# Performance work log

Measured on AMD Instinct MI355X. Metric: run time of the kernel, lower is better.

## Reference

```python
import jax, jax.numpy as jnp
import numpy as np
import math

N, C, W, H = 8, 1024, 1024, 16
D = C // H  # head size = 64


def setup_inputs() -> dict:
    key = jax.random.key(0)
    ks = jax.random.split(key, 7)
    s = 1.0 / math.sqrt(C)
    return {
        "hidden_states": jax.random.normal(ks[0], (N, C, W), jnp.float32),
        "attention_mask": jnp.zeros((N, 1, 1, W), jnp.float32),
        "wq": jax.random.normal(ks[1], (C, C), jnp.float32) * s,
        "bq": jax.random.normal(ks[2], (C,), jnp.float32) * 0.02,
        "wk": jax.random.normal(ks[3], (C, C), jnp.float32) * s,
        "bk": jax.random.normal(ks[4], (C,), jnp.float32) * 0.02,
        "wv": jax.random.normal(ks[5], (C, C), jnp.float32) * s,
        "bv": jax.random.normal(ks[6], (C,), jnp.float32) * 0.02,
    }


def reference(hidden_states, attention_mask, wq, bq, wk, bk, wv, bv):
    # conv1d(kernel=1, groups=1) == per-position GEMM: [N,C,W] x [Cout,Cin] -> [N,Cout,W]
    q = jnp.einsum('ncw,oc->now', hidden_states, wq) + bq[None, :, None]
    k = jnp.einsum('ncw,oc->now', hidden_states, wk) + bk[None, :, None]
    v = jnp.einsum('ncw,oc->now', hidden_states, wv) + bv[None, :, None]
    # split heads: [N,C,W] -> [N,H,D,W]
    q = q.reshape(N, H, D, W).transpose(0, 1, 3, 2)  # [N,H,W,D]
    k = k.reshape(N, H, D, W)                         # [N,H,D,W]
    v = v.reshape(N, H, D, W).transpose(0, 1, 3, 2)  # [N,H,W,D]
    scores = jnp.einsum('nhqd,nhdk->nhqk', q, k) / math.sqrt(D)
    scores = scores + attention_mask  # broadcast [N,1,1,W]
    probs = jax.nn.softmax(scores, axis=-1)
    ctx = jnp.einsum('nhqk,nhkd->nhqd', probs, v)    # [N,H,W,D]
    # merge heads back to [N,C,W]
    return ctx.transpose(0, 1, 3, 2).reshape(N, C, W)
```

## Files before the change

kernel.cpp:

```cpp
#include <hip/hip_runtime.h>
#include <hip/hip_bf16.h>

typedef __bf16 bf16x8 __attribute__((ext_vector_type(8)));
typedef __bf16 bf16x4 __attribute__((ext_vector_type(4)));
typedef float f32x4 __attribute__((ext_vector_type(4)));

#define N_ 8
#define C_ 1024
#define W_ 1024
#define H_ 16
#define D_ 64

typedef __attribute__((address_space(3))) void lds_void;
typedef const __attribute__((address_space(1))) void gbl_void;
static __device__ __forceinline__ void gload_lds16(const void* g, void* l) {
    __builtin_amdgcn_global_load_lds((gbl_void*)g, (lds_void*)l, 16, 0, 0);
}

__global__ __launch_bounds__(256)
void convert_w(const float* __restrict__ s0, const float* __restrict__ s1,
               const float* __restrict__ s2, __bf16* __restrict__ dst) {
    const float* s = blockIdx.y == 0 ? s0 : (blockIdx.y == 1 ? s1 : s2);
    __bf16* d = dst + (long)blockIdx.y * C_ * C_;
    const long i = ((long)blockIdx.x * 256 + threadIdx.x) * 8;
    f32x4 a = *(const f32x4*)(const void*)(s + i);
    f32x4 b = *(const f32x4*)(const void*)(s + i + 4);
    bf16x8 v;
    #pragma unroll
    for (int t = 0; t < 4; ++t) { v[t] = (__bf16)a[t]; v[t + 4] = (__bf16)b[t]; }
    *(bf16x8*)(void*)(d + i) = v;
}

__global__ __launch_bounds__(256)
void transpose_x(const float* __restrict__ in, __bf16* __restrict__ outp) {
    __shared__ float tile[64][68];
    const long bin  = (long)blockIdx.z * C_ * W_;
    const long bout = (long)blockIdx.z * W_ * C_;
    const int w0 = blockIdx.x * 64, c0 = blockIdx.y * 64;
    const int t = threadIdx.x;
    const int rr = t >> 4;
    const int cg = (t & 15) * 4;
    #pragma unroll
    for (int it = 0; it < 4; ++it) {
        const int cr = it * 16 + rr;
        f32x4 v = *(const f32x4*)(const void*)(in + bin + (long)(c0 + cr) * W_ + w0 + cg);
        *(f32x4*)&tile[cr][cg] = v;
    }
    __syncthreads();
    #pragma unroll
    for (int it = 0; it < 4; ++it) {
        const int wr = it * 16 + rr;
        bf16x4 o;
        #pragma unroll
        for (int u = 0; u < 4; ++u) o[u] = (__bf16)tile[cg + u][wr];
        *(bf16x4*)(void*)(outp + bout + (long)(w0 + wr) * C_ + c0 + cg) = o;
    }
}

template<int OUT_T>
static __device__ __forceinline__
void gemm_body(const __bf16* __restrict__ Aw, const __bf16* __restrict__ Xn,
               const float* __restrict__ bias, __bf16* __restrict__ Pn,
               const int o0, const int w0,
               __bf16* __restrict__ As, __bf16* __restrict__ Bs) {
    constexpr int BK = 64;
    const int tid = threadIdx.x;
    const int wv = tid >> 6, lane = tid & 63;
    const int l15 = lane & 15, quad = lane >> 4;
    const int wr = (wv >> 1) * 64, wc = (wv & 1) * 64;
    const int lr8 = lane >> 3;
    const int lp = lane & 7;

    f32x4 acc[4][4] = {};

    for (int k0 = 0; k0 < C_; k0 += BK) {
        #pragma unroll
        for (int j = 0; j < 4; ++j) {
            const int seg = wv * 4 + j;
            const int r = seg * 8 + lr8;
            const int q = lp ^ (r & 7);
            gload_lds16(Aw + (long)(o0 + r) * C_ + k0 + q * 8, As + seg * 512);
            gload_lds16(Xn + (long)(w0 + r) * C_ + k0 + q * 8, Bs + seg * 512);
        }
        __syncthreads();
        bf16x8 af[4][2], bf[4][2];
        #pragma unroll
        for (int mt = 0; mt < 4; ++mt) {
            const int R = wr + mt * 16 + l15;
            #pragma unroll
            for (int s = 0; s < 2; ++s) {
                const int pos = (s * 4 + quad) ^ (R & 7);
                af[mt][s] = *(const bf16x8*)(const void*)&As[R * 64 + pos * 8];
            }
        }
        #pragma unroll
        for (int nt = 0; nt < 4; ++nt) {
            const int R = wc + nt * 16 + l15;
            #pragma unroll
            for (int s = 0; s < 2; ++s) {
                const int pos = (s * 4 + quad) ^ (R & 7);
                bf[nt][s] = *(const bf16x8*)(const void*)&Bs[R * 64 + pos * 8];
            }
        }
        #pragma unroll
        for (int s = 0; s < 2; ++s)
            #pragma unroll
            for (int mt = 0; mt < 4; ++mt)
                #pragma unroll
                for (int nt = 0; nt < 4; ++nt) {
                    if (OUT_T == 0)
                        acc[mt][nt] = __builtin_amdgcn_mfma_f32_16x16x32_bf16(af[mt][s], bf[nt][s], acc[mt][nt], 0, 0, 0);
                    else
                        acc[mt][nt] = __builtin_amdgcn_mfma_f32_16x16x32_bf16(bf[nt][s], af[mt][s], acc[mt][nt], 0, 0, 0);
                }
        __syncthreads();
    }

    #pragma unroll
    for (int mt = 0; mt < 4; ++mt) {
        #pragma unroll
        for (int nt = 0; nt < 4; ++nt) {
            #pragma unroll
            for (int rg = 0; rg < 4; ++rg) {
                if (OUT_T == 0) {
                    const int col = w0 + wc + nt * 16 + l15;
                    const int row = o0 + wr + mt * 16 + quad * 4 + rg;
                    Pn[(long)row * W_ + col] = (__bf16)(acc[mt][nt][rg] + bias[row]);
                } else {
                    const int o = o0 + wr + mt * 16 + l15;
                    const int w = w0 + wc + nt * 16 + quad * 4 + rg;
                    Pn[(long)w * C_ + o] = (__bf16)(acc[mt][nt][rg] + bias[o]);
                }
            }
        }
    }
}

__global__ __launch_bounds__(256)
void gemm_qkv(const __bf16* __restrict__ Wb, const __bf16* __restrict__ Xt,
              const float* __restrict__ bq, const float* __restrict__ bk,
              const float* __restrict__ bv,
              __bf16* __restrict__ Qt, __bf16* __restrict__ Kt,
              __bf16* __restrict__ Vb) {
    __shared__ __align__(16) __bf16 As[128 * 64];
    __shared__ __align__(16) __bf16 Bs[128 * 64];
    const int f = blockIdx.x;
    const int n = f & 7;
    const int j = f >> 3;
    const int which = j >> 6;
    const int t = j & 63;
    const int o0 = (t >> 3) * 128;
    const int w0 = (t & 7) * 128;
    const size_t SZ = (size_t)C_ * W_;
    const size_t WSZ = (size_t)C_ * C_;
    const __bf16* Xn = Xt + (size_t)n * SZ;
    const __bf16* Aw = Wb + (size_t)which * WSZ;
    if (which < 2)
        gemm_body<1>(Aw, Xn, which ? bk : bq, (which ? Kt : Qt) + n * SZ, o0, w0, As, Bs);
    else
        gemm_body<0>(Aw, Xn, bv, Vb + n * SZ, o0, w0, As, Bs);
}

__global__ __launch_bounds__(256)
void flash_attn(const __bf16* __restrict__ Qt,
                const __bf16* __restrict__ Kt,
                const __bf16* __restrict__ V,
                const float* __restrict__ mask,
                float* __restrict__ out) {
    __shared__ __align__(16) __bf16 Pl[4 * 16 * 64];
    __shared__ __align__(16) __bf16 Ks[2][64 * 64];
    __shared__ __align__(16) __bf16 Vs[2][64 * 64];

    const int f = blockIdx.x;
    const int g = (f & 7) + ((f >> 6) << 3);
    const int m = (f >> 3) & 7;
    const int n = g >> 4, h = g & 15;
    const int q0 = m * 128;

    const int tid = threadIdx.x;
    const int wave = tid >> 6, lane = tid & 63;
    const int l15 = lane & 15, quad = lane >> 4;
    const int lr8 = lane >> 3, lp = lane & 7;
    const long nqk = (long)n * W_ * C_;
    const long nv = (long)n * C_ * W_;
    const int hD = h * D_;
    const float* mrow = mask + (long)n * W_;
    constexpr float SC = 0.125f * 1.44269504f;
    constexpr float L2E = 1.44269504f;

    char* plb = (char*)Pl + wave * 2048;
    const int swz = (l15 & 7) << 4;
    const long plrow = l15 * 128;

    bf16x8 aq[2][2];
    #pragma unroll
    for (int qs = 0; qs < 2; ++qs)
        #pragma unroll
        for (int dc = 0; dc < 2; ++dc)
            aq[qs][dc] = *(const bf16x8*)(const void*)
                (Qt + nqk + (long)(q0 + wave * 32 + qs * 16 + l15) * C_ + hD + dc * 32 + quad * 8);

    f32x4 o_acc[2][4] = {};
    float l_ln[2] = {};

    auto stage = [&](int kt, int b) {
        #pragma unroll
        for (int jj = 0; jj < 2; ++jj) {
            const int seg = wave * 2 + jj;
            const int r = seg * 8 + lr8;
            const int q = lp ^ (r & 7);
            gload_lds16(Kt + nqk + (long)(kt + r) * C_ + hD + q * 8, &Ks[b][seg * 512]);
            gload_lds16(V + nv + (long)(hD + r) * W_ + kt + q * 8, &Vs[b][seg * 512]);
        }
    };

    stage(0, 0);

    for (int ti = 0; ti < W_ / 64; ++ti) {
        const int kt = ti * 64;
        const int cur = ti & 1;
        asm volatile("s_waitcnt vmcnt(0)" ::: "memory");
        __syncthreads();
        if (ti + 1 < W_ / 64) stage(kt + 64, cur ^ 1);

        bf16x8 bk[4][2], bv[4][2];
        #pragma unroll
        for (int ks = 0; ks < 4; ++ks)
            #pragma unroll
            for (int dc = 0; dc < 2; ++dc) {
                const int R = ks * 16 + l15;
                const int pos = (dc * 4 + quad) ^ (R & 7);
                bk[ks][dc] = *(const bf16x8*)(const void*)&Ks[cur][R * 64 + pos * 8];
            }
        #pragma unroll
        for (int ds = 0; ds < 4; ++ds)
            #pragma unroll
            for (int kc = 0; kc < 2; ++kc) {
                const int R = ds * 16 + l15;
                const int pos = (kc * 4 + quad) ^ (R & 7);
                bv[ds][kc] = *(const bf16x8*)(const void*)&Vs[cur][R * 64 + pos * 8];
            }
        f32x4 mk[4];
        #pragma unroll
        for (int ks = 0; ks < 4; ++ks)
            mk[ks] = *(const f32x4*)(const void*)(mrow + kt + ks * 16 + quad * 4);

        #pragma unroll
        for (int qs = 0; qs < 2; ++qs) {
            f32x4 s[4] = {};
            #pragma unroll
            for (int ks = 0; ks < 4; ++ks)
                #pragma unroll
                for (int dc = 0; dc < 2; ++dc)
                    s[ks] = __builtin_amdgcn_mfma_f32_16x16x32_bf16(bk[ks][dc], aq[qs][dc], s[ks], 0, 0, 0);
            #pragma unroll
            for (int ks = 0; ks < 4; ++ks) {
                #pragma unroll
                for (int rg = 0; rg < 4; ++rg)
                    s[ks][rg] = __builtin_exp2f(s[ks][rg] * SC + mk[ks][rg] * L2E);
                l_ln[qs] += (s[ks][0] + s[ks][1]) + (s[ks][2] + s[ks][3]);
            }
            #pragma unroll
            for (int ks = 0; ks < 4; ++ks) {
                bf16x4 p4;
                #pragma unroll
                for (int rg = 0; rg < 4; ++rg) p4[rg] = (__bf16)s[ks][rg];
                *(bf16x4*)(void*)(plb + plrow + (((ks * 32 + quad * 8) ^ swz))) = p4;
            }
            bf16x8 ap[2];
            #pragma unroll
            for (int kc = 0; kc < 2; ++kc)
                ap[kc] = *(const bf16x8*)(const void*)(plb + plrow + (((kc * 64 + quad * 16) ^ swz)));
            #pragma unroll
            for (int ds = 0; ds < 4; ++ds)
                #pragma unroll
                for (int kc = 0; kc < 2; ++kc)
                    o_acc[qs][ds] = __builtin_amdgcn_mfma_f32_16x16x32_bf16(ap[kc], bv[ds][kc], o_acc[qs][ds], 0, 0, 0);
        }
    }

    #pragma unroll
    for (int qs = 0; qs < 2; ++qs) {
        float l = l_ln[qs];
        l += __shfl_xor(l, 16, 64);
        l += __shfl_xor(l, 32, 64);
        const float linv = 1.0f / l;
        #pragma unroll
        for (int rg = 0; rg < 4; ++rg) {
            const float inv = __shfl(linv, quad * 4 + rg, 64);
            #pragma unroll
            for (int ds = 0; ds < 4; ++ds)
                out[nv + (long)(hD + ds * 16 + l15) * W_ + q0 + wave * 32 + qs * 16 + quad * 4 + rg]
                    = o_acc[qs][ds][rg] * inv;
        }
    }
}

extern "C" void kernel_launch(void* const* d_in, const int* in_sizes, int n_in,
                              void* d_out, int out_size, void* d_ws, size_t ws_size,
                              hipStream_t stream) {
    (void)in_sizes; (void)n_in; (void)out_size; (void)ws_size;
    const float* hs   = (const float*)d_in[0];
    const float* mask = (const float*)d_in[1];
    const float* wq   = (const float*)d_in[2];
    const float* bq   = (const float*)d_in[3];
    const float* wk   = (const float*)d_in[4];
    const float* bk   = (const float*)d_in[5];
    const float* wv   = (const float*)d_in[6];
    const float* bv   = (const float*)d_in[7];
    float* out = (float*)d_out;

    const size_t SZ = (size_t)N_ * C_ * W_;
    const size_t WSZ = (size_t)C_ * C_;
    __bf16* Wb = (__bf16*)d_ws;
    __bf16* Xt = Wb + 3 * WSZ;
    __bf16* Qt = Xt + SZ;
    __bf16* Kt = Qt + SZ;
    __bf16* Vb = Kt + SZ;

    convert_w<<<dim3(512, 3), 256, 0, stream>>>(wq, wk, wv, Wb);
    transpose_x<<<dim3(W_ / 64, C_ / 64, N_), 256, 0, stream>>>(hs, Xt);

    gemm_qkv<<<dim3(1536), 256, 0, stream>>>(Wb, Xt, bq, bk, bv, Qt, Kt, Vb);

    flash_attn<<<dim3(1024), 256, 0, stream>>>(Qt, Kt, Vb, mask, out);
}
```

Measured before the change: 248.7 us.

## Double-buffer QKV GEMM, merge prep kernels, reorder flash-attn softmax stages

Three separate changes. The weight-convert and input-transpose launches are merged into one prep kernel to save a launch. The QKV GEMM now uses a BK=32 double-buffered LDS pipeline with a 4-way swizzle, so the next tile's global loads overlap the current MFMAs. In flash attention, both query sub-tiles are processed in separate phases (all QK MFMAs, then exp, then P staging, then PV), the mask is pre-scaled by log2e, and exp2 uses the amdgcn builtin. The smaller K step doubles the number of barriers, and holding both sub-tiles' scores at once raises register pressure.

Result: faster. 235.5 us (-5.3%).

```diff
diff --git a/kernel.cpp b/kernel.cpp
--- a/kernel.cpp
+++ b/kernel.cpp
@@ -18,42 +18,48 @@
 }
 
 __global__ __launch_bounds__(256)
-void convert_w(const float* __restrict__ s0, const float* __restrict__ s1,
-               const float* __restrict__ s2, __bf16* __restrict__ dst) {
-    const float* s = blockIdx.y == 0 ? s0 : (blockIdx.y == 1 ? s1 : s2);
-    __bf16* d = dst + (long)blockIdx.y * C_ * C_;
-    const long i = ((long)blockIdx.x * 256 + threadIdx.x) * 8;
-    f32x4 a = *(const f32x4*)(const void*)(s + i);
-    f32x4 b = *(const f32x4*)(const void*)(s + i + 4);
-    bf16x8 v;
-    #pragma unroll
-    for (int t = 0; t < 4; ++t) { v[t] = (__bf16)a[t]; v[t + 4] = (__bf16)b[t]; }
-    *(bf16x8*)(void*)(d + i) = v;
-}
-
-__global__ __launch_bounds__(256)
-void transpose_x(const float* __restrict__ in, __bf16* __restrict__ outp) {
+void prep(const float* __restrict__ hs,
+          const float* __restrict__ wq, const float* __restrict__ wk,
+          const float* __restrict__ wv,
+          __bf16* __restrict__ Xt, __bf16* __restrict__ Wb) {
     __shared__ float tile[64][68];
-    const long bin  = (long)blockIdx.z * C_ * W_;
-    const long bout = (long)blockIdx.z * W_ * C_;
-    const int w0 = blockIdx.x * 64, c0 = blockIdx.y * 64;
+    const int b = blockIdx.x;
     const int t = threadIdx.x;
-    const int rr = t >> 4;
-    const int cg = (t & 15) * 4;
-    #pragma unroll
-    for (int it = 0; it < 4; ++it) {
-        const int cr = it * 16 + rr;
-        f32x4 v = *(const f32x4*)(const void*)(in + bin + (long)(c0 + cr) * W_ + w0 + cg);
-        *(f32x4*)&tile[cr][cg] = v;
-    }
-    __syncthreads();
-    #pragma unroll
-    for (int it = 0; it < 4; ++it) {
-        const int wr = it * 16 + rr;
-        bf16x4 o;
-        #pragma unroll
-        for (int u = 0; u < 4; ++u) o[u] = (__bf16)tile[cg + u][wr];
-        *(bf16x4*)(void*)(outp + bout + (long)(w0 + wr) * C_ + c0 + cg) = o;
+    if (b < 2048) {
+        const int bx = b & 15, by = (b >> 4) & 15, bz = b >> 8;
+        const long bin  = (long)bz * C_ * W_;
+        const long bout = (long)bz * W_ * C_;
+        const int w0 = bx * 64, c0 = by * 64;
+        const int rr = t >> 4;
+        const int cg = (t & 15) * 4;
+        #pragma unroll
+        for (int it = 0; it < 4; ++it) {
+            const int cr = it * 16 + rr;
+            f32x4 v = *(const f32x4*)(const void*)(hs + bin + (long)(c0 + cr) * W_ + w0 + cg);
+            *(f32x4*)&tile[cr][cg] = v;
+        }
+        __syncthreads();
+        #pragma unroll
+        for (int it = 0; it < 4; ++it) {
+            const int wr = it * 16 + rr;
+            bf16x4 o;
+            #pragma unroll
+            for (int u = 0; u < 4; ++u) o[u] = (__bf16)tile[cg + u][wr];
+            *(bf16x4*)(void*)(Xt + bout + (long)(w0 + wr) * C_ + c0 + cg) = o;
+        }
+    } else {
+        const int cb = b - 2048;
+        const int wsel = cb >> 9;
+        const int x = cb & 511;
+        const float* s = wsel == 0 ? wq : (wsel == 1 ? wk : wv);
+        __bf16* d = Wb + (long)wsel * C_ * C_;
+        const long i = ((long)x * 256 + t) * 8;
+        f32x4 a = *(const f32x4*)(const void*)(s + i);
+        f32x4 bb = *(const f32x4*)(const void*)(s + i + 4);
+        bf16x8 v;
+        #pragma unroll
+        for (int u = 0; u < 4; ++u) { v[u] = (__bf16)a[u]; v[u + 4] = (__bf16)bb[u]; }
+        *(bf16x8*)(void*)(d + i) = v;
     }
 }
 
@@ -63,56 +69,59 @@
                const float* __restrict__ bias, __bf16* __restrict__ Pn,
                const int o0, const int w0,
                __bf16* __restrict__ As, __bf16* __restrict__ Bs) {
-    constexpr int BK = 64;
     const int tid = threadIdx.x;
     const int wv = tid >> 6, lane = tid & 63;
     const int l15 = lane & 15, quad = lane >> 4;
     const int wr = (wv >> 1) * 64, wc = (wv & 1) * 64;
-    const int lr8 = lane >> 3;
-    const int lp = lane & 7;
+    const int lr4 = lane >> 2;
+    const int lc4 = lane & 3;
 
     f32x4 acc[4][4] = {};
 
-    for (int k0 = 0; k0 < C_; k0 += BK) {
-        #pragma unroll
-        for (int j = 0; j < 4; ++j) {
-            const int seg = wv * 4 + j;
-            const int r = seg * 8 + lr8;
-            const int q = lp ^ (r & 7);
-            gload_lds16(Aw + (long)(o0 + r) * C_ + k0 + q * 8, As + seg * 512);
-            gload_lds16(Xn + (long)(w0 + r) * C_ + k0 + q * 8, Bs + seg * 512);
-        }
-        __syncthreads();
-        bf16x8 af[4][2], bf[4][2];
+    auto stage = [&](int k0, int b) {
+        #pragma unroll
+        for (int j = 0; j < 2; ++j) {
+            const int seg = wv * 2 + j;
+            const int r = seg * 16 + lr4;
+            const int q = lc4 ^ (r & 3);
+            gload_lds16(Aw + (long)(o0 + r) * C_ + k0 + q * 8, As + b * 4096 + seg * 512);
+            gload_lds16(Xn + (long)(w0 + r) * C_ + k0 + q * 8, Bs + b * 4096 + seg * 512);
+        }
+    };
+
+    stage(0, 0);
+    asm volatile("s_waitcnt vmcnt(0)" ::: "memory");
+    __syncthreads();
+
+    for (int ti = 0; ti < 32; ++ti) {
+        const int cur = ti & 1;
+        if (ti + 1 < 32) stage((ti + 1) * 32, cur ^ 1);
+
+        const __bf16* Ab = As + cur * 4096;
+        const __bf16* Bb = Bs + cur * 4096;
+        bf16x8 af[4], bf[4];
         #pragma unroll
         for (int mt = 0; mt < 4; ++mt) {
             const int R = wr + mt * 16 + l15;
-            #pragma unroll
-            for (int s = 0; s < 2; ++s) {
-                const int pos = (s * 4 + quad) ^ (R & 7);
-                af[mt][s] = *(const bf16x8*)(const void*)&As[R * 64 + pos * 8];
-            }
+            const int pos = quad ^ (R & 3);
+            af[mt] = *(const bf16x8*)(const void*)&Ab[R * 32 + pos * 8];
         }
         #pragma unroll
         for (int nt = 0; nt < 4; ++nt) {
             const int R = wc + nt * 16 + l15;
-            #pragma unroll
-            for (int s = 0; s < 2; ++s) {
-                const int pos = (s * 4 + quad) ^ (R & 7);
-                bf[nt][s] = *(const bf16x8*)(const void*)&Bs[R * 64 + pos * 8];
-            }
-        }
-        #pragma unroll
-        for (int s = 0; s < 2; ++s)
-            #pragma unroll
-            for (int mt = 0; mt < 4; ++mt)
-                #pragma unroll
-                for (int nt = 0; nt < 4; ++nt) {
-                    if (OUT_T == 0)
-                        acc[mt][nt] = __builtin_amdgcn_mfma_f32_16x16x32_bf16(af[mt][s], bf[nt][s], acc[mt][nt], 0, 0, 0);
-                    else
-                        acc[mt][nt] = __builtin_amdgcn_mfma_f32_16x16x32_bf16(bf[nt][s], af[mt][s], acc[mt][nt], 0, 0, 0);
-                }
+            const int pos = quad ^ (R & 3);
+            bf[nt] = *(const bf16x8*)(const void*)&Bb[R * 32 + pos * 8];
+        }
+        #pragma unroll
+        for (int mt = 0; mt < 4; ++mt)
+            #pragma unroll
+            for (int nt = 0; nt < 4; ++nt) {
+                if (OUT_T == 0)
+                    acc[mt][nt] = __builtin_amdgcn_mfma_f32_16x16x32_bf16(af[mt], bf[nt], acc[mt][nt], 0, 0, 0);
+                else
+                    acc[mt][nt] = __builtin_amdgcn_mfma_f32_16x16x32_bf16(bf[nt], af[mt], acc[mt][nt], 0, 0, 0);
+            }
+        asm volatile("s_waitcnt vmcnt(0)" ::: "memory");
         __syncthreads();
     }
 
@@ -142,8 +151,8 @@
               const float* __restrict__ bv,
               __bf16* __restrict__ Qt, __bf16* __restrict__ Kt,
               __bf16* __restrict__ Vb) {
-    __shared__ __align__(16) __bf16 As[128 * 64];
-    __shared__ __align__(16) __bf16 Bs[128 * 64];
+    __shared__ __align__(16) __bf16 As[2 * 4096];
+    __shared__ __align__(16) __bf16 Bs[2 * 4096];
     const int f = blockIdx.x;
     const int n = f & 7;
     const int j = f >> 3;
@@ -190,7 +199,7 @@
 
     char* plb = (char*)Pl + wave * 2048;
     const int swz = (l15 & 7) << 4;
-    const long plrow = l15 * 128;
+    const int plrow = l15 * 128;
 
     bf16x8 aq[2][2];
     #pragma unroll
@@ -223,7 +232,7 @@
         __syncthreads();
         if (ti + 1 < W_ / 64) stage(kt + 64, cur ^ 1);
 
-        bf16x8 bk[4][2], bv[4][2];
+        bf16x8 bk[4][2];
         #pragma unroll
         for (int ks = 0; ks < 4; ++ks)
             #pragma unroll
@@ -232,6 +241,50 @@
                 const int pos = (dc * 4 + quad) ^ (R & 7);
                 bk[ks][dc] = *(const bf16x8*)(const void*)&Ks[cur][R * 64 + pos * 8];
             }
+        f32x4 mk2[4];
+        #pragma unroll
+        for (int ks = 0; ks < 4; ++ks) {
+            f32x4 mv = *(const f32x4*)(const void*)(mrow + kt + ks * 16 + quad * 4);
+            #pragma unroll
+            for (int rg = 0; rg < 4; ++rg) mk2[ks][rg] = mv[rg] * L2E;
+        }
+
+        f32x4 s2[2][4] = {};
+        #pragma unroll
+        for (int qs = 0; qs < 2; ++qs)
+            #pragma unroll
+            for (int ks = 0; ks < 4; ++ks)
+                #pragma unroll
+                for (int dc = 0; dc < 2; ++dc)
+                    s2[qs][ks] = __builtin_amdgcn_mfma_f32_16x16x32_bf16(bk[ks][dc], aq[qs][dc], s2[qs][ks], 0, 0, 0);
+
+        #pragma unroll
+        for (int qs = 0; qs < 2; ++qs)
+            #pragma unroll
+            for (int ks = 0; ks < 4; ++ks) {
+                #pragma unroll
+                for (int rg = 0; rg < 4; ++rg)
+                    s2[qs][ks][rg] = __builtin_amdgcn_exp2f(s2[qs][ks][rg] * SC + mk2[ks][rg]);
+                l_ln[qs] += (s2[qs][ks][0] + s2[qs][ks][1]) + (s2[qs][ks][2] + s2[qs][ks][3]);
+            }
+
+        bf16x8 ap[2][2];
+        #pragma unroll
+        for (int qs = 0; qs < 2; ++qs) {
+            #pragma unroll
+            for (int ks = 0; ks < 4; ++ks) {
+                bf16x4 p4;
+                #pragma unroll
+                for (int rg = 0; rg < 4; ++rg) p4[rg] = (__bf16)s2[qs][ks][rg];
+                *(bf16x4*)(void*)(plb + plrow + ((ks * 32 + quad * 8) ^ swz)) = p4;
+            }
+            #pragma unroll
+            for (int kc = 0; kc < 2; ++kc)
+                ap[qs][kc] = *(const bf16x8*)(const void*)
+                    (plb + plrow + ((kc * 64 + quad * 16) ^ swz));
+        }
+
+        bf16x8 bv[4][2];
         #pragma unroll
         for (int ds = 0; ds < 4; ++ds)
             #pragma unroll
@@ -240,43 +293,13 @@
                 const int pos = (kc * 4 + quad) ^ (R & 7);
                 bv[ds][kc] = *(const bf16x8*)(const void*)&Vs[cur][R * 64 + pos * 8];
             }
-        f32x4 mk[4];
-        #pragma unroll
-        for (int ks = 0; ks < 4; ++ks)
-            mk[ks] = *(const f32x4*)(const void*)(mrow + kt + ks * 16 + quad * 4);
-
-        #pragma unroll
-        for (int qs = 0; qs < 2; ++qs) {
-            f32x4 s[4] = {};
-            #pragma unroll
-            for (int ks = 0; ks < 4; ++ks)
-                #pragma unroll
-                for (int dc = 0; dc < 2; ++dc)
-                    s[ks] = __builtin_amdgcn_mfma_f32_16x16x32_bf16(bk[ks][dc], aq[qs][dc], s[ks], 0, 0, 0);
-            #pragma unroll
-            for (int ks = 0; ks < 4; ++ks) {
-                #pragma unroll
-                for (int rg = 0; rg < 4; ++rg)
-                    s[ks][rg] = __builtin_exp2f(s[ks][rg] * SC + mk[ks][rg] * L2E);
-                l_ln[qs] += (s[ks][0] + s[ks][1]) + (s[ks][2] + s[ks][3]);
-            }
-            #pragma unroll
-            for (int ks = 0; ks < 4; ++ks) {
-                bf16x4 p4;
-                #pragma unroll
-                for (int rg = 0; rg < 4; ++rg) p4[rg] = (__bf16)s[ks][rg];
-                *(bf16x4*)(void*)(plb + plrow + (((ks * 32 + quad * 8) ^ swz))) = p4;
-            }
-            bf16x8 ap[2];
-            #pragma unroll
-            for (int kc = 0; kc < 2; ++kc)
-                ap[kc] = *(const bf16x8*)(const void*)(plb + plrow + (((kc * 64 + quad * 16) ^ swz)));
+        #pragma unroll
+        for (int qs = 0; qs < 2; ++qs)
             #pragma unroll
             for (int ds = 0; ds < 4; ++ds)
                 #pragma unroll
                 for (int kc = 0; kc < 2; ++kc)
-                    o_acc[qs][ds] = __builtin_amdgcn_mfma_f32_16x16x32_bf16(ap[kc], bv[ds][kc], o_acc[qs][ds], 0, 0, 0);
-        }
+                    o_acc[qs][ds] = __builtin_amdgcn_mfma_f32_16x16x32_bf16(ap[qs][kc], bv[ds][kc], o_acc[qs][ds], 0, 0, 0);
     }
 
     #pragma unroll
@@ -318,8 +341,7 @@
     __bf16* Kt = Qt + SZ;
     __bf16* Vb = Kt + SZ;
 
-    convert_w<<<dim3(512, 3), 256, 0, stream>>>(wq, wk, wv, Wb);
-    transpose_x<<<dim3(W_ / 64, C_ / 64, N_), 256, 0, stream>>>(hs, Xt);
+    prep<<<dim3(2048 + 1536), 256, 0, stream>>>(hs, wq, wk, wv, Xt, Wb);
 
     gemm_qkv<<<dim3(1536), 256, 0, stream>>>(Wb, Xt, bq, bk, bv, Qt, Kt, Vb);
 
```
